# Optimization experiments

Hardware: AMD Instinct MI355X
Metric: run time of the kernel (lower is better)

Reference implementation:

```python
import jax, jax.numpy as jnp
import numpy as np

EPS = 1e-06
ALPHA = 0.1
BETA = 0.1
B, N = 2048, 4096


def setup_inputs() -> dict:
    key = jax.random.key(0)
    k1, k2, k3, k4 = jax.random.split(key, 4)
    yhat = jax.random.normal(k1, (B, N), dtype=jnp.float32)
    y = jax.random.uniform(k2, (B, N), dtype=jnp.float32)
    batch_mask = jax.random.bernoulli(k3, 0.5, (B, N))
    # neighbor matrix: entries in {0, 1, 2} remapped to {0, alpha, beta}
    raw = jax.random.randint(k4, (N, N), 0, 3)
    spots_neighbors = jnp.where(raw == 1, ALPHA, jnp.where(raw == 2, BETA, 0.0)).astype(jnp.float32)
    return {"yhat": yhat, "y": y, "batch_mask": batch_mask, "spots_neighbors": spots_neighbors}


def reference(yhat, y, batch_mask, spots_neighbors):
    # squared error everywhere: [B, N]
    sq = jnp.square(y - yhat)
    # spatial_loss[:, i] = sq @ spots_neighbors[i]  ==  sq @ spots_neighbors.T
    spatial = jnp.einsum('bn,in->bi', sq, spots_neighbors)
    # masked_error at masked positions equals sq there, so total = sq + spatial, masked
    total = sq + spatial
    m = batch_mask.astype(sq.dtype)
    cnt = jnp.sum(m)
    loss = jnp.sqrt(jnp.sum(total * m) / cnt + EPS)
    return loss
```

## Files before the change

kernel.cpp:

```cpp
#include <hip/hip_runtime.h>
#include <hip/hip_bf16.h>

typedef int   i32x4  __attribute__((ext_vector_type(4)));
typedef int   i32x8  __attribute__((ext_vector_type(8)));
typedef float f32x16 __attribute__((ext_vector_type(16)));

#define BB 2048
#define NN 4096
#define NT 16

#define SQT_OFF ((size_t)0)
#define MT_OFF  ((size_t)16*1024*1024)
#define SCAL_OFF ((size_t)32*1024*1024)
#define PART_OFF (SCAL_OFF + 1024)
#define NBLK_P1 (64*32)

__device__ __forceinline__ unsigned f32_to_e4m3(float f) {
  if (f >= 448.0f) return 0x7eu;
  if (f < 0.015625f) return (unsigned)(int)rintf(f * 512.0f);
  unsigned u = __float_as_uint(f);
  unsigned r = u + 0x7ffffu + ((u >> 20) & 1u);
  int e = (int)((r >> 23) & 0xff) - 127;
  return ((unsigned)(e + 7) << 3) | ((r >> 20) & 7u);
}

__global__ void k_detect_zero(const unsigned char* __restrict__ mask,
                              float* __restrict__ scal, int* __restrict__ modep) {
  int lane = threadIdx.x;
  if (lane < 4) scal[lane] = 0.0f;
  bool h3f = false, oddnz = false;
  for (int i = 0; i < 64; ++i) {
    int idx = lane * 64 + i;
    unsigned char v = mask[idx];
    h3f |= (v == 0x3f);
    oddnz |= (((idx & 3) != 0) && (v != 0));
  }
  int mode = __any((int)h3f) ? 2 : (__any((int)oddnz) ? 0 : 1);
  if (lane == 0) *modep = mode;
}

struct P1Acc { float s1, cnt; };

template<int MODE>
__device__ __forceinline__ P1Acc p1_load_phase(
    const float* __restrict__ yhat, const float* __restrict__ y,
    const void* __restrict__ maskraw, unsigned short (*tile)[66],
    int b0, int n0, int brw, int nq)
{
  float4 yv[4], hv[4];
  float mv[4][4];
  #pragma unroll
  for (int rr = 0; rr < 4; ++rr) {
    int brow = brw + rr * 16;
    size_t idx = (size_t)(b0 + brow) * NN + n0 + nq;
    yv[rr] = *(const float4*)(y + idx);
    hv[rr] = *(const float4*)(yhat + idx);
    if (MODE == 0) {
      uchar4 t = *(const uchar4*)((const unsigned char*)maskraw + idx);
      mv[rr][0] = (float)t.x; mv[rr][1] = (float)t.y;
      mv[rr][2] = (float)t.z; mv[rr][3] = (float)t.w;
    } else if (MODE == 1) {
      int4 t = *(const int4*)((const int*)maskraw + idx);
      mv[rr][0] = (t.x != 0) ? 1.f : 0.f; mv[rr][1] = (t.y != 0) ? 1.f : 0.f;
      mv[rr][2] = (t.z != 0) ? 1.f : 0.f; mv[rr][3] = (t.w != 0) ? 1.f : 0.f;
    } else {
      float4 t = *(const float4*)((const float*)maskraw + idx);
      mv[rr][0] = (t.x != 0.f) ? 1.f : 0.f; mv[rr][1] = (t.y != 0.f) ? 1.f : 0.f;
      mv[rr][2] = (t.z != 0.f) ? 1.f : 0.f; mv[rr][3] = (t.w != 0.f) ? 1.f : 0.f;
    }
  }
  float s1 = 0.f, cnt = 0.f;
  #pragma unroll
  for (int rr = 0; rr < 4; ++rr) {
    int brow = brw + rr * 16;
    float d0 = yv[rr].x - hv[rr].x, d1 = yv[rr].y - hv[rr].y;
    float d2 = yv[rr].z - hv[rr].z, d3 = yv[rr].w - hv[rr].w;
    float sq[4] = { d0*d0, d1*d1, d2*d2, d3*d3 };
    unsigned t0 = f32_to_e4m3(sq[0]) | (mv[rr][0] != 0.f ? 0x3800u : 0u);
    unsigned t1 = f32_to_e4m3(sq[1]) | (mv[rr][1] != 0.f ? 0x3800u : 0u);
    unsigned t2 = f32_to_e4m3(sq[2]) | (mv[rr][2] != 0.f ? 0x3800u : 0u);
    unsigned t3 = f32_to_e4m3(sq[3]) | (mv[rr][3] != 0.f ? 0x3800u : 0u);
    *(uint2*)(&tile[brow][nq]) = make_uint2(t0 | (t1 << 16), t2 | (t3 << 16));
    s1 += sq[0]*mv[rr][0] + sq[1]*mv[rr][1] + sq[2]*mv[rr][2] + sq[3]*mv[rr][3];
    cnt += mv[rr][0] + mv[rr][1] + mv[rr][2] + mv[rr][3];
  }
  return { s1, cnt };
}

__global__ __launch_bounds__(256, 2) void k_pass1(
    const float* __restrict__ yhat, const float* __restrict__ y,
    const void* __restrict__ maskraw,
    unsigned char* __restrict__ SQT, unsigned char* __restrict__ MT,
    float2* __restrict__ part, const int* __restrict__ modep)
{
  __shared__ unsigned short tile[64][66];
  __shared__ float red[8];
  const int mode = *modep;
  const int tid = threadIdx.x;
  const int n0 = blockIdx.x * 64;
  const int b0 = blockIdx.y * 64;
  const int nq = (tid & 15) * 4;
  const int brw = tid >> 4;
  P1Acc a;
  if (mode == 0)      a = p1_load_phase<0>(yhat, y, maskraw, tile, b0, n0, brw, nq);
  else if (mode == 1) a = p1_load_phase<1>(yhat, y, maskraw, tile, b0, n0, brw, nq);
  else                a = p1_load_phase<2>(yhat, y, maskraw, tile, b0, n0, brw, nq);
  __syncthreads();
  {
    int nrow = tid >> 2;
    int cb   = tid & 3;
    int grow = n0 + nrow;
    unsigned x = (unsigned)((grow & 7) << 4);
    unsigned us[4], um[4];
    #pragma unroll
    for (int q = 0; q < 4; ++q) {
      unsigned v0 = tile[cb*16 + q*4 + 0][nrow];
      unsigned v1 = tile[cb*16 + q*4 + 1][nrow];
      unsigned v2 = tile[cb*16 + q*4 + 2][nrow];
      unsigned v3 = tile[cb*16 + q*4 + 3][nrow];
      us[q] = (v0 & 0xffu) | ((v1 & 0xffu) << 8) | ((v2 & 0xffu) << 16) | ((v3 & 0xffu) << 24);
      um[q] = (v0 >> 8) | ((v1 >> 8) << 8) | ((v2 >> 8) << 16) | ((v3 >> 8) << 24);
    }
    unsigned Bb = (unsigned)(b0 + cb * 16);
    unsigned pos = (Bb & ~127u) | ((Bb & 127u) ^ x);
    size_t base = (size_t)grow * BB;
    *(uint4*)(SQT + base + pos) = make_uint4(us[0], us[1], us[2], us[3]);
    *(uint4*)(MT  + base + pos) = make_uint4(um[0], um[1], um[2], um[3]);
  }
  float s1 = a.s1, cnt = a.cnt;
  #pragma unroll
  for (int off = 32; off >= 1; off >>= 1) {
    s1  += __shfl_down(s1,  off, 64);
    cnt += __shfl_down(cnt, off, 64);
  }
  int wv = tid >> 6;
  if ((tid & 63) == 0) { red[wv] = s1; red[4 + wv] = cnt; }
  __syncthreads();
  if (tid == 0)
    part[blockIdx.y * gridDim.x + blockIdx.x] =
        make_float2(red[0] + red[1] + red[2] + red[3],
                    red[4] + red[5] + red[6] + red[7]);
}

__global__ __launch_bounds__(512, 2) void k_gemm(
    const unsigned char* __restrict__ MT,
    const unsigned char* __restrict__ SQT,
    const float* __restrict__ W,
    float* __restrict__ scal)
{
  extern __shared__ char lds[];
  const int tid = threadIdx.x;
  const int lane = tid & 63;
  const int wave = tid >> 6;
  const int wm = wave >> 2;
  const int wn = wave & 3;
  const int l31 = lane & 31;
  const int lh32 = (lane >> 5) * 32;
  const int wmB = wm * 128, wnB = wn * 64;

  int bid = blockIdx.x;
  int swz = (bid & 7) * 32 + (bid >> 3);
  const int n0 = (swz & 15) * 256;
  const int i0 = (swz >> 4) * 256;

  const size_t aOff = (size_t)(i0 + (tid >> 3)) * BB + (tid & 7) * 16;
  const size_t bOff = (size_t)(n0 + (tid >> 3)) * BB + (tid & 7) * 16;
  const int tid16 = tid * 16;

#define STG_A(buf, inst, ktv) \
  __builtin_amdgcn_global_load_lds( \
      (const __attribute__((address_space(1))) unsigned int*)(MT + aOff + (size_t)(inst)*64*BB + (ktv)), \
      (__attribute__((address_space(3))) unsigned int*)(lds + (buf)*32768 + (inst)*8192 + tid16), 16, 0, 0)
#define STG_B(buf, inst, ktv) \
  __builtin_amdgcn_global_load_lds( \
      (const __attribute__((address_space(1))) unsigned int*)(SQT + bOff + (size_t)(inst)*64*BB + (ktv)), \
      (__attribute__((address_space(3))) unsigned int*)(lds + 65536 + (buf)*32768 + (inst)*8192 + tid16), 16, 0, 0)

  i32x8 a0[4], a1[4], b0v[2], b1v[2];

#define RD_A(dst, base, KH) \
  _Pragma("unroll") for (int mg = 0; mg < 4; ++mg) { \
    int r = wmB + mg * 32 + l31; \
    int x = (r & 7) << 4; \
    const char* rp = (base) + r * 128; \
    int o = (KH) * 64 + lh32; \
    i32x4 lo = *(const i32x4*)(rp + (o ^ x)); \
    i32x4 hi = *(const i32x4*)(rp + ((o + 16) ^ x)); \
    dst[mg] = __builtin_shufflevector(lo, hi, 0, 1, 2, 3, 4, 5, 6, 7); \
  }
#define RD_B(dst, base, KH) \
  _Pragma("unroll") for (int ng = 0; ng < 2; ++ng) { \
    int r = wnB + ng * 32 + l31; \
    int x = (r & 7) << 4; \
    const char* rp = (base) + r * 128; \
    int o = (KH) * 64 + lh32; \
    i32x4 lo = *(const i32x4*)(rp + (o ^ x)); \
    i32x4 hi = *(const i32x4*)(rp + ((o + 16) ^ x)); \
    dst[ng] = __builtin_shufflevector(lo, hi, 0, 1, 2, 3, 4, 5, 6, 7); \
  }
#define MFMA_H(AS, BS) \
  __builtin_amdgcn_s_setprio(1); \
  _Pragma("unroll") for (int mg = 0; mg < 4; ++mg) \
    _Pragma("unroll") for (int ng = 0; ng < 2; ++ng) \
      acc[mg][ng] = __builtin_amdgcn_mfma_scale_f32_32x32x64_f8f6f4( \
          AS[mg], BS[ng], acc[mg][ng], 0, 0, 0, 0x7f7f7f7f, 0, 0x7f7f7f7f); \
  __builtin_amdgcn_s_setprio(0); \
  __builtin_amdgcn_s_barrier(); \
  __builtin_amdgcn_sched_barrier(0)

  STG_A(0,0,0); STG_A(0,1,0); STG_A(0,2,0); STG_A(0,3,0);
  STG_B(0,0,0); STG_B(0,1,0); STG_B(0,2,0); STG_B(0,3,0);
  STG_A(1,0,128); STG_A(1,1,128); STG_A(1,2,128); STG_A(1,3,128);
  STG_B(1,0,128); STG_B(1,1,128); STG_B(1,2,128); STG_B(1,3,128);
  asm volatile("s_waitcnt vmcnt(8)" ::: "memory");
  __builtin_amdgcn_s_barrier();
  __builtin_amdgcn_sched_barrier(0);

  f32x16 acc[4][2] = {};

  RD_A(a0, lds, 0);
  RD_B(b0v, lds + 65536, 0);

  for (int t = 0; t < NT; ++t) {
    const char* bAc = lds + (t & 1) * 32768;
    const char* bBc = lds + 65536 + (t & 1) * 32768;
    const char* bAn = lds + ((t + 1) & 1) * 32768;
    const char* bBn = lds + 65536 + ((t + 1) & 1) * 32768;
    const int sb = t & 1;
    const int ktv = (t + 2) * 128;
    const bool st = (t + 2) < NT;
    const bool rn = (t + 1) < NT;

    RD_A(a1, bAc, 1);
    RD_B(b1v, bBc, 1);
    MFMA_H(a0, b0v);

    if (st) {
      STG_A(sb, 0, ktv); STG_A(sb, 1, ktv); STG_A(sb, 2, ktv); STG_A(sb, 3, ktv);
      STG_B(sb, 0, ktv); STG_B(sb, 1, ktv); STG_B(sb, 2, ktv); STG_B(sb, 3, ktv);
      asm volatile("s_waitcnt vmcnt(8)" ::: "memory");
    } else {
      asm volatile("s_waitcnt vmcnt(0)" ::: "memory");
    }
    if (rn) { RD_A(a0, bAn, 0); RD_B(b0v, bBn, 0); }
    MFMA_H(a1, b1v);
  }
#undef STG_A
#undef STG_B
#undef RD_A
#undef RD_B
#undef MFMA_H

  float local = 0.0f;
  #pragma unroll
  for (int mg = 0; mg < 4; ++mg) {
    int rbase = i0 + wmB + mg * 32 + (lane >> 5) * 4;
    #pragma unroll
    for (int ng = 0; ng < 2; ++ng) {
      int nn = n0 + wnB + ng * 32 + l31;
      const float* wp = W + (size_t)rbase * NN + nn;
      #pragma unroll
      for (int reg = 0; reg < 16; ++reg) {
        int roff = (reg & 3) + 8 * (reg >> 2);
        local += acc[mg][ng][reg] * wp[(size_t)roff * NN];
      }
    }
  }
  #pragma unroll
  for (int off = 32; off >= 1; off >>= 1)
    local += __shfl_down(local, off, 64);
  float* wpart = (float*)lds;
  if (lane == 0) wpart[wave] = local;
  __builtin_amdgcn_s_barrier();
  if (tid == 0) {
    float s = 0.f;
    #pragma unroll
    for (int i = 0; i < 8; ++i) s += wpart[i];
    atomicAdd(&scal[2], s);
  }
}

__global__ __launch_bounds__(256) void k_finalize(
    const float2* __restrict__ part, const float* __restrict__ scal,
    float* __restrict__ out)
{
  __shared__ float rs[4], rc[4];
  float s1 = 0.f, cnt = 0.f;
  for (int i = threadIdx.x; i < NBLK_P1; i += 256) {
    float2 p = part[i];
    s1 += p.x; cnt += p.y;
  }
  #pragma unroll
  for (int off = 32; off >= 1; off >>= 1) {
    s1  += __shfl_down(s1,  off, 64);
    cnt += __shfl_down(cnt, off, 64);
  }
  int wv = threadIdx.x >> 6;
  if ((threadIdx.x & 63) == 0) { rs[wv] = s1; rc[wv] = cnt; }
  __syncthreads();
  if (threadIdx.x == 0) {
    float S = rs[0] + rs[1] + rs[2] + rs[3];
    float C = rc[0] + rc[1] + rc[2] + rc[3];
    out[0] = sqrtf((S + scal[2]) / C + 1e-6f);
  }
}

__global__ void k_sentinel(float* out) { out[0] = 1.2345e8f; }

extern "C" void kernel_launch(void* const* d_in, const int* in_sizes, int n_in,
                              void* d_out, int out_size, void* d_ws, size_t ws_size,
                              hipStream_t stream) {
  const float* yhat = (const float*)d_in[0];
  const float* y    = (const float*)d_in[1];
  const void*  mask = d_in[2];
  const float* W    = (const float*)d_in[3];
  float* out = (float*)d_out;

  const size_t need = PART_OFF + (size_t)NBLK_P1 * 8;
  if (ws_size < need) { k_sentinel<<<1, 1, 0, stream>>>(out); return; }

  char* ws = (char*)d_ws;
  unsigned char* SQT = (unsigned char*)(ws + SQT_OFF);
  unsigned char* MTp = (unsigned char*)(ws + MT_OFF);
  float* scal = (float*)(ws + SCAL_OFF);
  int* modep  = (int*)(ws + SCAL_OFF + 16);
  float2* part = (float2*)(ws + PART_OFF);

  (void)hipFuncSetAttribute((const void*)k_gemm,
                            hipFuncAttributeMaxDynamicSharedMemorySize, 131072);

  k_detect_zero<<<1, 64, 0, stream>>>((const unsigned char*)mask, scal, modep);
  k_pass1<<<dim3(NN/64, BB/64), 256, 0, stream>>>(yhat, y, mask, SQT, MTp, part, modep);
  k_gemm<<<256, 512, 131072, stream>>>(MTp, SQT, W, scal);
  k_finalize<<<1, 256, 0, stream>>>(part, scal, out);
}
```

Before: 73.56 us.

## Shrink GEMM tiles to 128x128, pre-tile FP8 operands, drop atomic accumulation

The fp8 GEMM moves from 256x256 tiles (256 blocks) to 128x128 tiles (1024 blocks) with 64 KB of LDS, so more blocks can be resident per CU and the 256-CU device is better filled. Pass1 now writes SQT and MT in a blocked layout of 128-row by 128-k tiles, each split into 16-byte chunks, so every k-step is one contiguous 16 KB region per operand. LDS staging and reads therefore become linear with no XOR swizzle. The atomicAdd into a shared scalar is replaced by per-block partials that the finalize kernel sums. Smaller tiles halve the data reuse per block, which raises L2 and global traffic and adds MFMA issue overhead per byte loaded.

```diff
diff --git a/kernel.cpp b/kernel.cpp
--- a/kernel.cpp
+++ b/kernel.cpp
@@ -13,7 +13,9 @@
 #define MT_OFF  ((size_t)16*1024*1024)
 #define SCAL_OFF ((size_t)32*1024*1024)
 #define PART_OFF (SCAL_OFF + 1024)
+#define PART2_OFF (PART_OFF + 16384)
 #define NBLK_P1 (64*32)
+#define NBLK_G  1024
 
 __device__ __forceinline__ unsigned f32_to_e4m3(float f) {
   if (f >= 448.0f) return 0x7eu;
@@ -110,7 +112,6 @@
     int nrow = tid >> 2;
     int cb   = tid & 3;
     int grow = n0 + nrow;
-    unsigned x = (unsigned)((grow & 7) << 4);
     unsigned us[4], um[4];
     #pragma unroll
     for (int q = 0; q < 4; ++q) {
@@ -121,11 +122,11 @@
       us[q] = (v0 & 0xffu) | ((v1 & 0xffu) << 8) | ((v2 & 0xffu) << 16) | ((v3 & 0xffu) << 24);
       um[q] = (v0 >> 8) | ((v1 >> 8) << 8) | ((v2 >> 8) << 16) | ((v3 >> 8) << 24);
     }
-    unsigned Bb = (unsigned)(b0 + cb * 16);
-    unsigned pos = (Bb & ~127u) | ((Bb & 127u) ^ x);
-    size_t base = (size_t)grow * BB;
-    *(uint4*)(SQT + base + pos) = make_uint4(us[0], us[1], us[2], us[3]);
-    *(uint4*)(MT  + base + pos) = make_uint4(um[0], um[1], um[2], um[3]);
+    int gb = b0 + cb * 16;
+    size_t off = (size_t)(grow >> 7) * 262144 + (size_t)(gb >> 7) * 16384
+               + (size_t)((gb >> 4) & 7) * 2048 + (size_t)(grow & 127) * 16;
+    *(uint4*)(SQT + off) = make_uint4(us[0], us[1], us[2], us[3]);
+    *(uint4*)(MT  + off) = make_uint4(um[0], um[1], um[2], um[3]);
   }
   float s1 = a.s1, cnt = a.cnt;
   #pragma unroll
@@ -142,107 +143,92 @@
                     red[4] + red[5] + red[6] + red[7]);
 }
 
-__global__ __launch_bounds__(512, 2) void k_gemm(
+__global__ __launch_bounds__(512, 4) void k_gemm(
     const unsigned char* __restrict__ MT,
     const unsigned char* __restrict__ SQT,
     const float* __restrict__ W,
-    float* __restrict__ scal)
+    float* __restrict__ part2)
 {
   extern __shared__ char lds[];
   const int tid = threadIdx.x;
   const int lane = tid & 63;
   const int wave = tid >> 6;
-  const int wm = wave >> 2;
-  const int wn = wave & 3;
+  const int wmB = (wave >> 1) * 32;
+  const int wnB = (wave & 1) * 64;
   const int l31 = lane & 31;
-  const int lh32 = (lane >> 5) * 32;
-  const int wmB = wm * 128, wnB = wn * 64;
+  const int lch2 = (lane >> 5) * 2;
 
   int bid = blockIdx.x;
-  int swz = (bid & 7) * 32 + (bid >> 3);
-  const int n0 = (swz & 15) * 256;
-  const int i0 = (swz >> 4) * 256;
-
-  const size_t aOff = (size_t)(i0 + (tid >> 3)) * BB + (tid & 7) * 16;
-  const size_t bOff = (size_t)(n0 + (tid >> 3)) * BB + (tid & 7) * 16;
+  int swz = (bid & 7) * 128 + (bid >> 3);
+  const int nb = swz & 31, ib = swz >> 5;
+  const int n0 = nb * 128, i0 = ib * 128;
+
+  const unsigned char* aSrc = MT  + (size_t)ib * 262144;
+  const unsigned char* bSrc = SQT + (size_t)nb * 262144;
   const int tid16 = tid * 16;
 
-#define STG_A(buf, inst, ktv) \
-  __builtin_amdgcn_global_load_lds( \
-      (const __attribute__((address_space(1))) unsigned int*)(MT + aOff + (size_t)(inst)*64*BB + (ktv)), \
-      (__attribute__((address_space(3))) unsigned int*)(lds + (buf)*32768 + (inst)*8192 + tid16), 16, 0, 0)
-#define STG_B(buf, inst, ktv) \
-  __builtin_amdgcn_global_load_lds( \
-      (const __attribute__((address_space(1))) unsigned int*)(SQT + bOff + (size_t)(inst)*64*BB + (ktv)), \
-      (__attribute__((address_space(3))) unsigned int*)(lds + 65536 + (buf)*32768 + (inst)*8192 + tid16), 16, 0, 0)
-
-  i32x8 a0[4], a1[4], b0v[2], b1v[2];
-
-#define RD_A(dst, base, KH) \
-  _Pragma("unroll") for (int mg = 0; mg < 4; ++mg) { \
-    int r = wmB + mg * 32 + l31; \
-    int x = (r & 7) << 4; \
-    const char* rp = (base) + r * 128; \
-    int o = (KH) * 64 + lh32; \
-    i32x4 lo = *(const i32x4*)(rp + (o ^ x)); \
-    i32x4 hi = *(const i32x4*)(rp + ((o + 16) ^ x)); \
-    dst[mg] = __builtin_shufflevector(lo, hi, 0, 1, 2, 3, 4, 5, 6, 7); \
-  }
-#define RD_B(dst, base, KH) \
+#define STG_A(c, kt) \
+  { __builtin_amdgcn_global_load_lds( \
+      (const __attribute__((address_space(1))) unsigned int*)(aSrc + (size_t)(kt)*16384 + tid16), \
+      (__attribute__((address_space(3))) unsigned int*)(lds + (c)*16384 + tid16), 16, 0, 0); \
+    __builtin_amdgcn_global_load_lds( \
+      (const __attribute__((address_space(1))) unsigned int*)(aSrc + (size_t)(kt)*16384 + 8192 + tid16), \
+      (__attribute__((address_space(3))) unsigned int*)(lds + (c)*16384 + 8192 + tid16), 16, 0, 0); }
+#define STG_B(c, kt) \
+  { __builtin_amdgcn_global_load_lds( \
+      (const __attribute__((address_space(1))) unsigned int*)(bSrc + (size_t)(kt)*16384 + tid16), \
+      (__attribute__((address_space(3))) unsigned int*)(lds + 32768 + (c)*16384 + tid16), 16, 0, 0); \
+    __builtin_amdgcn_global_load_lds( \
+      (const __attribute__((address_space(1))) unsigned int*)(bSrc + (size_t)(kt)*16384 + 8192 + tid16), \
+      (__attribute__((address_space(3))) unsigned int*)(lds + 32768 + (c)*16384 + 8192 + tid16), 16, 0, 0); }
+
+#define RD_A(dst, c, kh) { \
+    const char* p = lds + (c)*16384 + ((kh)*4 + lch2)*2048 + (wmB + l31)*16; \
+    i32x4 lo = *(const i32x4*)p; \
+    i32x4 hi = *(const i32x4*)(p + 2048); \
+    dst = __builtin_shufflevector(lo, hi, 0, 1, 2, 3, 4, 5, 6, 7); }
+#define RD_B(dst, c, kh) \
   _Pragma("unroll") for (int ng = 0; ng < 2; ++ng) { \
-    int r = wnB + ng * 32 + l31; \
-    int x = (r & 7) << 4; \
-    const char* rp = (base) + r * 128; \
-    int o = (KH) * 64 + lh32; \
-    i32x4 lo = *(const i32x4*)(rp + (o ^ x)); \
-    i32x4 hi = *(const i32x4*)(rp + ((o + 16) ^ x)); \
-    dst[ng] = __builtin_shufflevector(lo, hi, 0, 1, 2, 3, 4, 5, 6, 7); \
-  }
+    const char* p = lds + 32768 + (c)*16384 + ((kh)*4 + lch2)*2048 + (wnB + ng*32 + l31)*16; \
+    i32x4 lo = *(const i32x4*)p; \
+    i32x4 hi = *(const i32x4*)(p + 2048); \
+    dst[ng] = __builtin_shufflevector(lo, hi, 0, 1, 2, 3, 4, 5, 6, 7); }
 #define MFMA_H(AS, BS) \
   __builtin_amdgcn_s_setprio(1); \
-  _Pragma("unroll") for (int mg = 0; mg < 4; ++mg) \
-    _Pragma("unroll") for (int ng = 0; ng < 2; ++ng) \
-      acc[mg][ng] = __builtin_amdgcn_mfma_scale_f32_32x32x64_f8f6f4( \
-          AS[mg], BS[ng], acc[mg][ng], 0, 0, 0, 0x7f7f7f7f, 0, 0x7f7f7f7f); \
+  _Pragma("unroll") for (int ng = 0; ng < 2; ++ng) \
+    acc[ng] = __builtin_amdgcn_mfma_scale_f32_32x32x64_f8f6f4( \
+        AS, BS[ng], acc[ng], 0, 0, 0, 0x7f7f7f7f, 0, 0x7f7f7f7f); \
   __builtin_amdgcn_s_setprio(0); \
   __builtin_amdgcn_s_barrier(); \
   __builtin_amdgcn_sched_barrier(0)
 
-  STG_A(0,0,0); STG_A(0,1,0); STG_A(0,2,0); STG_A(0,3,0);
-  STG_B(0,0,0); STG_B(0,1,0); STG_B(0,2,0); STG_B(0,3,0);
-  STG_A(1,0,128); STG_A(1,1,128); STG_A(1,2,128); STG_A(1,3,128);
-  STG_B(1,0,128); STG_B(1,1,128); STG_B(1,2,128); STG_B(1,3,128);
-  asm volatile("s_waitcnt vmcnt(8)" ::: "memory");
+  i32x8 a0, a1, b0v[2], b1v[2];
+  f32x16 acc[2] = {};
+
+  STG_A(0, 0); STG_B(0, 0);
+  STG_A(1, 1); STG_B(1, 1);
+  asm volatile("s_waitcnt vmcnt(4)" ::: "memory");
   __builtin_amdgcn_s_barrier();
   __builtin_amdgcn_sched_barrier(0);
-
-  f32x16 acc[4][2] = {};
-
-  RD_A(a0, lds, 0);
-  RD_B(b0v, lds + 65536, 0);
+  RD_A(a0, 0, 0);
+  RD_B(b0v, 0, 0);
 
   for (int t = 0; t < NT; ++t) {
-    const char* bAc = lds + (t & 1) * 32768;
-    const char* bBc = lds + 65536 + (t & 1) * 32768;
-    const char* bAn = lds + ((t + 1) & 1) * 32768;
-    const char* bBn = lds + 65536 + ((t + 1) & 1) * 32768;
-    const int sb = t & 1;
-    const int ktv = (t + 2) * 128;
+    const int c = t & 1, cn = c ^ 1;
     const bool st = (t + 2) < NT;
     const bool rn = (t + 1) < NT;
 
-    RD_A(a1, bAc, 1);
-    RD_B(b1v, bBc, 1);
+    RD_A(a1, c, 1);
+    RD_B(b1v, c, 1);
     MFMA_H(a0, b0v);
 
     if (st) {
-      STG_A(sb, 0, ktv); STG_A(sb, 1, ktv); STG_A(sb, 2, ktv); STG_A(sb, 3, ktv);
-      STG_B(sb, 0, ktv); STG_B(sb, 1, ktv); STG_B(sb, 2, ktv); STG_B(sb, 3, ktv);
-      asm volatile("s_waitcnt vmcnt(8)" ::: "memory");
+      STG_A(c, t + 2); STG_B(c, t + 2);
+      asm volatile("s_waitcnt vmcnt(4)" ::: "memory");
     } else {
       asm volatile("s_waitcnt vmcnt(0)" ::: "memory");
     }
-    if (rn) { RD_A(a0, bAn, 0); RD_B(b0v, bBn, 0); }
+    if (rn) { RD_A(a0, cn, 0); RD_B(b0v, cn, 0); }
     MFMA_H(a1, b1v);
   }
 #undef STG_A
@@ -252,9 +238,8 @@
 #undef MFMA_H
 
   float local = 0.0f;
-  #pragma unroll
-  for (int mg = 0; mg < 4; ++mg) {
-    int rbase = i0 + wmB + mg * 32 + (lane >> 5) * 4;
+  {
+    int rbase = i0 + wmB + (lane >> 5) * 4;
     #pragma unroll
     for (int ng = 0; ng < 2; ++ng) {
       int nn = n0 + wnB + ng * 32 + l31;
@@ -262,7 +247,7 @@
       #pragma unroll
       for (int reg = 0; reg < 16; ++reg) {
         int roff = (reg & 3) + 8 * (reg >> 2);
-        local += acc[mg][ng][reg] * wp[(size_t)roff * NN];
+        local += acc[ng][reg] * wp[(size_t)roff * NN];
       }
     }
   }
@@ -276,12 +261,12 @@
     float s = 0.f;
     #pragma unroll
     for (int i = 0; i < 8; ++i) s += wpart[i];
-    atomicAdd(&scal[2], s);
+    part2[blockIdx.x] = s;
   }
 }
 
 __global__ __launch_bounds__(256) void k_finalize(
-    const float2* __restrict__ part, const float* __restrict__ scal,
+    const float2* __restrict__ part, const float* __restrict__ part2,
     float* __restrict__ out)
 {
   __shared__ float rs[4], rc[4];
@@ -290,6 +275,8 @@
     float2 p = part[i];
     s1 += p.x; cnt += p.y;
   }
+  for (int i = threadIdx.x; i < NBLK_G; i += 256)
+    s1 += part2[i];
   #pragma unroll
   for (int off = 32; off >= 1; off >>= 1) {
     s1  += __shfl_down(s1,  off, 64);
@@ -301,7 +288,7 @@
   if (threadIdx.x == 0) {
     float S = rs[0] + rs[1] + rs[2] + rs[3];
     float C = rc[0] + rc[1] + rc[2] + rc[3];
-    out[0] = sqrtf((S + scal[2]) / C + 1e-6f);
+    out[0] = sqrtf(S / C + 1e-6f);
   }
 }
 
@@ -316,7 +303,7 @@
   const float* W    = (const float*)d_in[3];
   float* out = (float*)d_out;
 
-  const size_t need = PART_OFF + (size_t)NBLK_P1 * 8;
+  const size_t need = PART2_OFF + (size_t)NBLK_G * 4;
   if (ws_size < need) { k_sentinel<<<1, 1, 0, stream>>>(out); return; }
 
   char* ws = (char*)d_ws;
@@ -325,12 +312,13 @@
   float* scal = (float*)(ws + SCAL_OFF);
   int* modep  = (int*)(ws + SCAL_OFF + 16);
   float2* part = (float2*)(ws + PART_OFF);
+  float* part2 = (float*)(ws + PART2_OFF);
 
   (void)hipFuncSetAttribute((const void*)k_gemm,
-                            hipFuncAttributeMaxDynamicSharedMemorySize, 131072);
+                            hipFuncAttributeMaxDynamicSharedMemorySize, 65536);
 
   k_detect_zero<<<1, 64, 0, stream>>>((const unsigned char*)mask, scal, modep);
   k_pass1<<<dim3(NN/64, BB/64), 256, 0, stream>>>(yhat, y, mask, SQT, MTp, part, modep);
-  k_gemm<<<256, 512, 131072, stream>>>(MTp, SQT, W, scal);
-  k_finalize<<<1, 256, 0, stream>>>(part, scal, out);
-}
+  k_gemm<<<NBLK_G, 512, 65536, stream>>>(MTp, SQT, W, part2);
+  k_finalize<<<1, 256, 0, stream>>>(part, part2, out);
+}
```

Result: slower. 77.41 us (+5.2%).
